# Optimization experiments

Hardware: AMD Instinct MI355X
Metric: run time of the kernel (lower is better)

The kernel has to match this reference:

```python
import jax, jax.numpy as jnp
import numpy as np

H = 8       # num_heads
D = 64      # inner_dim (per-head)
DM = 512    # input_dim == output_dim
EPS = 1e-5


def setup_inputs() -> dict:
    key = jax.random.key(0)
    ks = jax.random.split(key, 6)
    b, n = 2, 2048
    x = jax.random.normal(ks[0], (b, n, DM), dtype=jnp.float32)
    w_qkv = jax.random.normal(ks[1], (DM, 3 * H * D), dtype=jnp.float32) * (DM ** -0.5)
    head_mix = jax.random.normal(ks[2], (H, H), dtype=jnp.float32)
    ln_h_g = jnp.ones((H,), jnp.float32)
    ln_h_b = jnp.zeros((H,), jnp.float32)
    w_out = jax.random.normal(ks[3], (H * D, DM), dtype=jnp.float32) * ((H * D) ** -0.5)
    b_out = jnp.zeros((DM,), jnp.float32)
    ln_o_g = jnp.ones((DM,), jnp.float32)
    ln_o_b = jnp.zeros((DM,), jnp.float32)
    return {"x": x, "w_qkv": w_qkv, "head_mix": head_mix,
            "ln_h_g": ln_h_g, "ln_h_b": ln_h_b,
            "w_out": w_out, "b_out": b_out,
            "ln_o_g": ln_o_g, "ln_o_b": ln_o_b}


def reference(x, w_qkv, head_mix, ln_h_g, ln_h_b, w_out, b_out, ln_o_g, ln_o_b):
    b, n, _ = x.shape
    scale = D ** -0.5
    qkv = x @ w_qkv                                   # [b, n, 3*H*D]
    q, k, v = jnp.split(qkv, 3, axis=-1)
    def heads(t):
        return t.reshape(b, n, H, D).transpose(0, 2, 1, 3)  # [b, H, n, D]
    q, k, v = heads(q), heads(k), heads(v)
    dots = jnp.einsum('bhid,bhjd->bhij', q, k) * scale
    attn = jax.nn.softmax(dots, axis=-1)
    # talking-heads mix: bhij,hg->bgij
    attn = jnp.einsum('bhij,hg->bgij', attn, head_mix)
    # LayerNorm over the head axis (axis=1)
    mu = attn.mean(axis=1, keepdims=True)
    var = attn.var(axis=1, keepdims=True)
    attn = (attn - mu) * jax.lax.rsqrt(var + EPS)
    attn = attn * ln_h_g[None, :, None, None] + ln_h_b[None, :, None, None]
    out = jnp.einsum('bhij,bhjd->bhid', attn, v)      # [b, H, n, D]
    out = out.transpose(0, 2, 1, 3).reshape(b, n, H * D)
    out = out @ w_out + b_out                         # [b, n, DM]
    # LayerNorm over feature dim
    mo = out.mean(axis=-1, keepdims=True)
    vo = out.var(axis=-1, keepdims=True)
    out = (out - mo) * jax.lax.rsqrt(vo + EPS) * ln_o_g + ln_o_b
    out = (x + out).sum(axis=1)                       # [b, DM]
    return out, attn
```

## Files before the change

kernel.cpp:

```cpp
#include <hip/hip_runtime.h>
#include <hip/hip_bf16.h>

typedef __attribute__((ext_vector_type(8)))  short short8;
typedef __attribute__((ext_vector_type(16))) float f32x16;

#define LOG2E 1.44269504088896f
#define CS (0.125f * LOG2E)

static __device__ __forceinline__ short f2b(float f) {
  union { __hip_bfloat16 h; short s; } u; u.h = __float2bfloat16(f); return u.s;
}
static __device__ __forceinline__ f32x16 zf16() {
  f32x16 z;
#pragma unroll
  for (int i = 0; i < 16; ++i) z[i] = 0.f;
  return z;
}
static __device__ __forceinline__ f32x16 mfma32(short8 a, short8 b, f32x16 c) {
  return __builtin_amdgcn_mfma_f32_32x32x16_bf16(a, b, c, 0, 0, 0);
}
static __device__ __forceinline__ float rfl(float v) {
  return __int_as_float(__builtin_amdgcn_readfirstlane(__float_as_int(v)));
}

__global__ void k_convert(const float* __restrict__ x, const float* __restrict__ wqkv,
                          const float* __restrict__ wout,
                          short* __restrict__ xb, short* __restrict__ wqkvT,
                          short* __restrict__ woutT) {
  const int NX = 2 * 2048 * 512;
  const int NW = 512 * 1536;
  const int NO = 512 * 512;
  int i = blockIdx.x * 256 + threadIdx.x;
  if (i < NX) {
    xb[i] = f2b(x[i]);
  } else if (i < NX + NW) {
    int o = i - NX; int n = o >> 9; int k = o & 511;
    wqkvT[o] = f2b(wqkv[k * 1536 + n]);
  } else if (i < NX + NW + NO) {
    int o = i - NX - NW; int n = o >> 9; int k = o & 511;
    woutT[o] = f2b(wout[k * 512 + n]);
  }
}

__global__ void k_xsum(const float* __restrict__ x, float* __restrict__ outacc) {
  int blk = blockIdx.x;
  int b = blk >> 4, ch = blk & 15;
  int t = threadIdx.x;
  int f = t * 2;
  float s0 = 0.f, s1 = 0.f;
  const float* base = x + ((size_t)b * 2048 + (size_t)ch * 128) * 512;
  for (int r = 0; r < 128; ++r) {
    float2 v = *(const float2*)(base + (size_t)r * 512 + f);
    s0 += v.x; s1 += v.y;
  }
  atomicAdd(&outacc[b * 512 + f], s0);
  atomicAdd(&outacc[b * 512 + f + 1], s1);
}

__launch_bounds__(256)
__global__ void k_qkv(const short* __restrict__ xb, const short* __restrict__ wqkvT,
                      short* __restrict__ qg, short* __restrict__ kg,
                      short* __restrict__ vtmp) {
  __shared__ __align__(16) short As[128 * 64];
  __shared__ __align__(16) short Bs[128 * 64];
  int bx = blockIdx.x & 31;
  int by = blockIdx.x >> 5;
  int row0 = bx << 7, col0 = by << 7;
  int t = threadIdx.x, w = t >> 6, l = t & 63, li = l & 31, hi = l >> 5;
  int wr = w >> 1, wc = w & 1;
  f32x16 acc[2][2];
#pragma unroll
  for (int mi = 0; mi < 2; ++mi)
#pragma unroll
    for (int ni = 0; ni < 2; ++ni) acc[mi][ni] = zf16();

  for (int k0 = 0; k0 < 512; k0 += 64) {
    __syncthreads();
#pragma unroll
    for (int it = 0; it < 4; ++it) {
      int idx = t + it * 256;
      int r = idx >> 3, pc = idx & 7;
      int4 va = *(const int4*)(xb + (size_t)(row0 + r) * 512 + k0 + pc * 8);
      int dsto = (r * 128 + pc * 16) ^ ((r & 7) << 4);
      *(int4*)((char*)As + dsto) = va;
      int4 vb = *(const int4*)(wqkvT + (size_t)(col0 + r) * 512 + k0 + pc * 8);
      *(int4*)((char*)Bs + dsto) = vb;
    }
    __syncthreads();
#pragma unroll
    for (int kk = 0; kk < 4; ++kk) {
      short8 af[2], bfv[2];
#pragma unroll
      for (int mi = 0; mi < 2; ++mi) {
        int row = wr * 64 + mi * 32 + li;
        int byteo = (row * 128 + (kk * 2 + hi) * 16) ^ ((row & 7) << 4);
        af[mi] = *(const short8*)((char*)As + byteo);
      }
#pragma unroll
      for (int ni = 0; ni < 2; ++ni) {
        int col = wc * 64 + ni * 32 + li;
        int byteo = (col * 128 + (kk * 2 + hi) * 16) ^ ((col & 7) << 4);
        bfv[ni] = *(const short8*)((char*)Bs + byteo);
      }
#pragma unroll
      for (int mi = 0; mi < 2; ++mi)
#pragma unroll
        for (int ni = 0; ni < 2; ++ni)
          acc[mi][ni] = mfma32(af[mi], bfv[ni], acc[mi][ni]);
    }
  }
#pragma unroll
  for (int mi = 0; mi < 2; ++mi)
#pragma unroll
    for (int ni = 0; ni < 2; ++ni) {
      int colb = col0 + wc * 64 + ni * 32 + li;
      int sect = colb >> 9, rem = colb & 511, h = rem >> 6, d = rem & 63;
      short* dst = sect == 0 ? qg : (sect == 1 ? kg : vtmp);
#pragma unroll
      for (int r = 0; r < 16; ++r) {
        int row = row0 + wr * 64 + mi * 32 + ((r & 3) + ((r >> 2) << 3) + (hi << 2));
        int b = row >> 11, nn = row & 2047;
        dst[(((size_t)(b * 8 + h) * 2048 + nn) << 6) + d] = f2b(acc[mi][ni][r]);
      }
    }
}

__global__ void k_vt(const short* __restrict__ vtmp, short* __restrict__ vt) {
  __shared__ __align__(16) short tile[64 * 72];
  int blk = blockIdx.x;
  int bh = blk >> 5;
  int n0 = (blk & 31) << 6;
  int t = threadIdx.x;
#pragma unroll
  for (int it = 0; it < 2; ++it) {
    int idx = (t + it * 256) * 8;
    int r = idx >> 6, c = idx & 63;
    int4 v = *(const int4*)(vtmp + ((size_t)bh * 2048 + n0 + r) * 64 + c);
    *(int4*)(&tile[r * 72 + c]) = v;
  }
  __syncthreads();
#pragma unroll
  for (int it = 0; it < 2; ++it) {
    int idx = (t + it * 256) * 8;
    int d = idx >> 6, nn = idx & 63;
    short8 o;
#pragma unroll
    for (int j = 0; j < 8; ++j) o[j] = tile[(nn + j) * 72 + d];
    *(short8*)(vt + ((size_t)bh * 64 + d) * 2048 + n0 + nn) = o;
  }
}

__launch_bounds__(256)
__global__ void k_stats(const short* __restrict__ qg, const short* __restrict__ kg,
                        float* __restrict__ ml) {
  __shared__ float red[4][32][2];
  int t = threadIdx.x, w = t >> 6, l = t & 63, li = l & 31, hi = l >> 5;
  int blk = blockIdx.x;
  int b = blk >> 9, rem = blk & 511, h = rem >> 6, it = rem & 63;
  size_t bh = (size_t)(b * 8 + h) * 2048;
  int i = it * 32 + li;
  short8 q4[4];
#pragma unroll
  for (int kk = 0; kk < 4; ++kk)
    q4[kk] = *(const short8*)(qg + (bh + i) * 64 + kk * 16 + hi * 8);
  float m2 = -1e30f, ls = 0.f;
  for (int jt = w * 16; jt < w * 16 + 16; ++jt) {
    f32x16 s = zf16();
#pragma unroll
    for (int kk = 0; kk < 4; ++kk) {
      short8 kf = *(const short8*)(kg + (bh + jt * 32 + li) * 64 + kk * 16 + hi * 8);
      s = mfma32(kf, q4[kk], s);
    }
    float sv[16];
    float tm = -1e30f;
#pragma unroll
    for (int r = 0; r < 16; ++r) { sv[r] = s[r] * CS; tm = fmaxf(tm, sv[r]); }
    float mn = fmaxf(m2, tm);
    float acc = 0.f;
#pragma unroll
    for (int r = 0; r < 16; ++r) acc += exp2f(sv[r] - mn);
    ls = ls * exp2f(m2 - mn) + acc;
    m2 = mn;
  }
  float om = __shfl_xor(m2, 32, 64);
  float ol = __shfl_xor(ls, 32, 64);
  float mf = fmaxf(m2, om);
  float lf = ls * exp2f(m2 - mf) + ol * exp2f(om - mf);
  if (hi == 0) { red[w][li][0] = mf; red[w][li][1] = lf; }
  __syncthreads();
  if (t < 32) {
    float m = red[0][t][0], s = red[0][t][1];
#pragma unroll
    for (int ww = 1; ww < 4; ++ww) {
      float m1 = red[ww][t][0], s1 = red[ww][t][1];
      float mn = fmaxf(m, m1);
      s = s * exp2f(m - mn) + s1 * exp2f(m1 - mn);
      m = mn;
    }
    *(float2*)(ml + (bh + it * 32 + t) * 2) = make_float2(m, s);
  }
}

__launch_bounds__(512, 4)
__global__ void k_attn(const short* __restrict__ qg, const short* __restrict__ kg,
                       const short* __restrict__ vt, const float* __restrict__ ml,
                       const float* __restrict__ mixg, const float* __restrict__ lnhg,
                       const float* __restrict__ lnhb, float* __restrict__ attn,
                       float* __restrict__ oh) {
  __shared__ __align__(16) float p_lds[8 * 32 * 33];
  __shared__ __align__(16) short a_lds[8 * 32 * 40];
  int t = threadIdx.x;
  int w = t >> 6, l = t & 63, li = l & 31, hi = l >> 5;
  int blk = blockIdx.x;
  int jg = blk & 3, itile = (blk >> 2) & 63, b = blk >> 8;
  int i0 = itile * 32;
  int h = w;
  size_t bh = (size_t)(b * 8 + h) * 2048;

  float mixr[64];
#pragma unroll
  for (int z = 0; z < 64; ++z) mixr[z] = rfl(mixg[z]);
  float lg[8], lbv[8];
#pragma unroll
  for (int g = 0; g < 8; ++g) { lg[g] = rfl(lnhg[g]); lbv[g] = rfl(lnhb[g]); }

  short8 q4[4];
#pragma unroll
  for (int kk = 0; kk < 4; ++kk)
    q4[kk] = *(const short8*)(qg + (bh + i0 + li) * 64 + kk * 16 + hi * 8);
  float2 mlv = *(const float2*)(ml + (bh + i0 + li) * 2);
  float c0 = -(mlv.x + __log2f(mlv.y));

  f32x16 oacc[2];
  oacc[0] = zf16(); oacc[1] = zf16();

  int ii = t >> 4;
  int jp = (t & 15) * 2;

  for (int jt = 0; jt < 16; ++jt) {
    int j0 = jg * 512 + jt * 32;
    f32x16 s = zf16();
#pragma unroll
    for (int kk = 0; kk < 4; ++kk) {
      short8 kf = *(const short8*)(kg + (bh + j0 + li) * 64 + kk * 16 + hi * 8);
      s = mfma32(kf, q4[kk], s);
    }
#pragma unroll
    for (int r = 0; r < 16; ++r) {
      float p = exp2f(fmaf(s[r], CS, c0));
      int jr = (r & 3) + ((r >> 2) << 3) + (hi << 2);
      p_lds[(h * 32 + jr) * 33 + li] = p;
    }
    __syncthreads();
    {
      float pf[8][2], a[8][2];
#pragma unroll
      for (int g = 0; g < 8; ++g) {
        pf[g][0] = p_lds[(g * 32 + jp) * 33 + ii];
        pf[g][1] = p_lds[(g * 32 + jp + 1) * 33 + ii];
      }
#pragma unroll
      for (int g = 0; g < 8; ++g) {
#pragma unroll
        for (int jb = 0; jb < 2; ++jb) {
          float a2 = 0.f;
#pragma unroll
          for (int hh = 0; hh < 8; ++hh) a2 = fmaf(pf[hh][jb], mixr[hh * 8 + g], a2);
          a[g][jb] = a2;
        }
      }
      float mu[2], rs[2];
#pragma unroll
      for (int jb = 0; jb < 2; ++jb) {
        float m2 = 0.f;
#pragma unroll
        for (int g = 0; g < 8; ++g) m2 += a[g][jb];
        m2 *= 0.125f;
        float var = 0.f;
#pragma unroll
        for (int g = 0; g < 8; ++g) { float d2 = a[g][jb] - m2; var = fmaf(d2, d2, var); }
        var *= 0.125f;
        mu[jb] = m2; rs[jb] = rsqrtf(var + 1e-5f);
      }
#pragma unroll
      for (int g = 0; g < 8; ++g) {
        float y0 = (a[g][0] - mu[0]) * rs[0] * lg[g] + lbv[g];
        float y1 = (a[g][1] - mu[1]) * rs[1] * lg[g] + lbv[g];
        *(float2*)(&attn[((size_t)(b * 8 + g) * 2048 + (size_t)(i0 + ii)) * 2048 + j0 + jp]) =
            make_float2(y0, y1);
        unsigned int pk = (unsigned short)f2b(y0) | ((unsigned int)(unsigned short)f2b(y1) << 16);
        *(unsigned int*)(&a_lds[(g * 32 + ii) * 40 + jp]) = pk;
      }
    }
    __syncthreads();
#pragma unroll
    for (int ks = 0; ks < 2; ++ks) {
      short8 af = *(const short8*)(&a_lds[(h * 32 + li) * 40 + ks * 16 + hi * 8]);
#pragma unroll
      for (int dt = 0; dt < 2; ++dt) {
        short8 vf = *(const short8*)(vt + ((size_t)(b * 8 + h) * 64 + dt * 32 + li) * 2048 + j0 + ks * 16 + hi * 8);
        oacc[dt] = mfma32(af, vf, oacc[dt]);
      }
    }
  }
  float* ohp = oh + (size_t)jg * (2 * 2048 * 512);
#pragma unroll
  for (int dt = 0; dt < 2; ++dt)
#pragma unroll
    for (int r = 0; r < 16; ++r) {
      int ri = (r & 3) + ((r >> 2) << 3) + (hi << 2);
      ohp[((size_t)(b * 2048 + i0 + ri)) * 512 + h * 64 + dt * 32 + li] = oacc[dt][r];
    }
}

__launch_bounds__(512)
__global__ void k_epi(const float* __restrict__ oh, const short* __restrict__ woutT,
                      const float* __restrict__ bo, const float* __restrict__ logv,
                      const float* __restrict__ lob, float* __restrict__ dout) {
  __shared__ __align__(16) short As[32 * 64];
  __shared__ float lnsum[32][8];
  __shared__ float lnsq[32][8];
  __shared__ float zsum[512];
  const size_t NPART = (size_t)2 * 2048 * 512;
  int t = threadIdx.x, w = t >> 6, l = t & 63, li = l & 31, hi = l >> 5;
  int m0 = blockIdx.x * 32;
  f32x16 acc[2];
  acc[0] = zf16(); acc[1] = zf16();

  for (int k0 = 0; k0 < 512; k0 += 64) {
    __syncthreads();
    {
      int r = t >> 4, c = (t & 15) * 4;
      size_t off = (size_t)(m0 + r) * 512 + k0 + c;
      float4 v = *(const float4*)(oh + off);
#pragma unroll
      for (int p = 1; p < 4; ++p) {
        float4 v2 = *(const float4*)(oh + p * NPART + off);
        v.x += v2.x; v.y += v2.y; v.z += v2.z; v.w += v2.w;
      }
      short o[4] = { f2b(v.x), f2b(v.y), f2b(v.z), f2b(v.w) };
      int byteo = (r * 128 + c * 2) ^ ((r & 7) << 4);
      *(int2*)((char*)As + byteo) = *(int2*)o;
    }
    __syncthreads();
#pragma unroll
    for (int kk = 0; kk < 4; ++kk) {
      int byteo = (li * 128 + (kk * 2 + hi) * 16) ^ ((li & 7) << 4);
      short8 af = *(const short8*)((char*)As + byteo);
#pragma unroll
      for (int ni = 0; ni < 2; ++ni) {
        int n = w * 64 + ni * 32 + li;
        short8 bfr = *(const short8*)(woutT + (size_t)n * 512 + k0 + kk * 16 + hi * 8);
        acc[ni] = mfma32(af, bfr, acc[ni]);
      }
    }
  }
  float bias[2], gg[2], b2[2];
#pragma unroll
  for (int ni = 0; ni < 2; ++ni) {
    int n = w * 64 + ni * 32 + li;
    bias[ni] = bo[n]; gg[ni] = logv[n]; b2[ni] = lob[n];
  }
#pragma unroll
  for (int ni = 0; ni < 2; ++ni)
#pragma unroll
    for (int r = 0; r < 16; ++r) acc[ni][r] += bias[ni];

#pragma unroll
  for (int r = 0; r < 16; ++r) {
    float s = acc[0][r] + acc[1][r];
    float q2 = fmaf(acc[0][r], acc[0][r], acc[1][r] * acc[1][r]);
    for (int d2 = 1; d2 < 32; d2 <<= 1) { s += __shfl_xor(s, d2); q2 += __shfl_xor(q2, d2); }
    int row = (r & 3) + ((r >> 2) << 3) + (hi << 2);
    if (li == 0) { lnsum[row][w] = s; lnsq[row][w] = q2; }
  }
  __syncthreads();
  if (t < 32) {
    float s = 0.f, q2 = 0.f;
#pragma unroll
    for (int ww = 0; ww < 8; ++ww) { s += lnsum[t][ww]; q2 += lnsq[t][ww]; }
    float m2 = s * (1.f / 512.f);
    float var = q2 * (1.f / 512.f) - m2 * m2;
    lnsum[t][0] = m2;
    lnsq[t][0] = rsqrtf(var + 1e-5f);
  }
  __syncthreads();
  float zc[2] = {0.f, 0.f};
#pragma unroll
  for (int r = 0; r < 16; ++r) {
    int row = (r & 3) + ((r >> 2) << 3) + (hi << 2);
    float m2 = lnsum[row][0], rs = lnsq[row][0];
#pragma unroll
    for (int ni = 0; ni < 2; ++ni)
      zc[ni] += (acc[ni][r] - m2) * rs * gg[ni] + b2[ni];
  }
#pragma unroll
  for (int ni = 0; ni < 2; ++ni) zc[ni] += __shfl_xor(zc[ni], 32);
  if (hi == 0) {
#pragma unroll
    for (int ni = 0; ni < 2; ++ni) zsum[w * 64 + ni * 32 + li] = zc[ni];
  }
  __syncthreads();
  int bsel = m0 >> 11;
  atomicAdd(&dout[bsel * 512 + t], zsum[t]);
}

extern "C" void kernel_launch(void* const* d_in, const int* in_sizes, int n_in,
                              void* d_out, int out_size, void* d_ws, size_t ws_size,
                              hipStream_t stream) {
  const float* x    = (const float*)d_in[0];
  const float* wqkv = (const float*)d_in[1];
  const float* mixg = (const float*)d_in[2];
  const float* lnhg = (const float*)d_in[3];
  const float* lnhb = (const float*)d_in[4];
  const float* wout = (const float*)d_in[5];
  const float* bo   = (const float*)d_in[6];
  const float* logv = (const float*)d_in[7];
  const float* lob  = (const float*)d_in[8];
  float* dout = (float*)d_out;
  char* ws = (char*)d_ws;
  short* xb    = (short*)(ws + 0);
  short* wqkvT = (short*)(ws + 4194304);
  short* woutT = (short*)(ws + 5767168);
  short* qg    = (short*)(ws + 6291456);
  short* kg    = (short*)(ws + 10485760);
  short* vtmp  = (short*)(ws + 14680064);
  short* vt    = (short*)(ws + 18874368);
  float* ml    = (float*)(ws + 23068672);
  float* oh    = (float*)(ws + 23330816);

  hipMemsetAsync(dout, 0, 1024 * sizeof(float), stream);

  k_convert<<<12288, 256, 0, stream>>>(x, wqkv, wout, xb, wqkvT, woutT);
  k_xsum<<<32, 256, 0, stream>>>(x, dout);
  k_qkv<<<384, 256, 0, stream>>>(xb, wqkvT, qg, kg, vtmp);
  k_vt<<<512, 256, 0, stream>>>(vtmp, vt);
  k_stats<<<1024, 256, 0, stream>>>(qg, kg, ml);
  k_attn<<<512, 512, 0, stream>>>(qg, kg, vt, ml, mixg, lnhg, lnhb, dout + 1024, oh);
  k_epi<<<128, 512, 0, stream>>>(oh, woutT, bo, logv, lob, dout);
}
```

Baseline: 452.4 us.

## Compute talking-heads mix with MFMA on bf16 probabilities instead of scalar FMAs

Replaces the per-thread 8x8 scalar head-mixing (64 FMAs per element with 64 mix registers) with a 32x32x16 bf16 MFMA, where the mix matrix sits in the first 8 rows of the A operand and the probabilities are stored as bf16 in swizzled LDS. The head LayerNorm is then computed with a cross-half shuffle, and the occupancy hint in launch_bounds is dropped because register pressure should fall. The intent is to remove the VALU and register cost of the mix. In exchange, most of the MFMA work is zero padding, probabilities are rounded to bf16 before mixing, which loses precision, and the attn stores become scalar 4-byte writes instead of float2.

Result: slower. 493.2 us (+9.0%).

```diff
diff --git a/kernel.cpp b/kernel.cpp
--- a/kernel.cpp
+++ b/kernel.cpp
@@ -18,9 +18,6 @@
 }
 static __device__ __forceinline__ f32x16 mfma32(short8 a, short8 b, f32x16 c) {
   return __builtin_amdgcn_mfma_f32_32x32x16_bf16(a, b, c, 0, 0, 0);
-}
-static __device__ __forceinline__ float rfl(float v) {
-  return __int_as_float(__builtin_amdgcn_readfirstlane(__float_as_int(v)));
 }
 
 __global__ void k_convert(const float* __restrict__ x, const float* __restrict__ wqkv,
@@ -201,13 +198,13 @@
   }
 }
 
-__launch_bounds__(512, 4)
+__launch_bounds__(512)
 __global__ void k_attn(const short* __restrict__ qg, const short* __restrict__ kg,
                        const short* __restrict__ vt, const float* __restrict__ ml,
                        const float* __restrict__ mixg, const float* __restrict__ lnhg,
                        const float* __restrict__ lnhb, float* __restrict__ attn,
                        float* __restrict__ oh) {
-  __shared__ __align__(16) float p_lds[8 * 32 * 33];
+  __shared__ __align__(16) short p_lds[1024 * 8];
   __shared__ __align__(16) short a_lds[8 * 32 * 40];
   int t = threadIdx.x;
   int w = t >> 6, l = t & 63, li = l & 31, hi = l >> 5;
@@ -217,12 +214,13 @@
   int h = w;
   size_t bh = (size_t)(b * 8 + h) * 2048;
 
-  float mixr[64];
-#pragma unroll
-  for (int z = 0; z < 64; ++z) mixr[z] = rfl(mixg[z]);
-  float lg[8], lbv[8];
-#pragma unroll
-  for (int g = 0; g < 8; ++g) { lg[g] = rfl(lnhg[g]); lbv[g] = rfl(lnhb[g]); }
+  short8 mixA;
+#pragma unroll
+  for (int e = 0; e < 8; ++e)
+    mixA[e] = (hi == 0 && li < 8) ? f2b(mixg[e * 8 + li]) : (short)0;
+  float lg4[4], lb4[4];
+#pragma unroll
+  for (int e = 0; e < 4; ++e) { lg4[e] = lnhg[4 * hi + e]; lb4[e] = lnhb[4 * hi + e]; }
 
   short8 q4[4];
 #pragma unroll
@@ -234,9 +232,6 @@
   f32x16 oacc[2];
   oacc[0] = zf16(); oacc[1] = zf16();
 
-  int ii = t >> 4;
-  int jp = (t & 15) * 2;
-
   for (int jt = 0; jt < 16; ++jt) {
     int j0 = jg * 512 + jt * 32;
     f32x16 s = zf16();
@@ -249,47 +244,44 @@
     for (int r = 0; r < 16; ++r) {
       float p = exp2f(fmaf(s[r], CS, c0));
       int jr = (r & 3) + ((r >> 2) << 3) + (hi << 2);
-      p_lds[(h * 32 + jr) * 33 + li] = p;
-    }
-    __syncthreads();
-    {
-      float pf[8][2], a[8][2];
-#pragma unroll
-      for (int g = 0; g < 8; ++g) {
-        pf[g][0] = p_lds[(g * 32 + jp) * 33 + ii];
-        pf[g][1] = p_lds[(g * 32 + jp + 1) * 33 + ii];
-      }
-#pragma unroll
-      for (int g = 0; g < 8; ++g) {
-#pragma unroll
-        for (int jb = 0; jb < 2; ++jb) {
-          float a2 = 0.f;
-#pragma unroll
-          for (int hh = 0; hh < 8; ++hh) a2 = fmaf(pf[hh][jb], mixr[hh * 8 + g], a2);
-          a[g][jb] = a2;
-        }
-      }
-      float mu[2], rs[2];
-#pragma unroll
-      for (int jb = 0; jb < 2; ++jb) {
-        float m2 = 0.f;
-#pragma unroll
-        for (int g = 0; g < 8; ++g) m2 += a[g][jb];
-        m2 *= 0.125f;
-        float var = 0.f;
-#pragma unroll
-        for (int g = 0; g < 8; ++g) { float d2 = a[g][jb] - m2; var = fmaf(d2, d2, var); }
-        var *= 0.125f;
-        mu[jb] = m2; rs[jb] = rsqrtf(var + 1e-5f);
-      }
-#pragma unroll
-      for (int g = 0; g < 8; ++g) {
-        float y0 = (a[g][0] - mu[0]) * rs[0] * lg[g] + lbv[g];
-        float y1 = (a[g][1] - mu[1]) * rs[1] * lg[g] + lbv[g];
-        *(float2*)(&attn[((size_t)(b * 8 + g) * 2048 + (size_t)(i0 + ii)) * 2048 + j0 + jp]) =
-            make_float2(y0, y1);
-        unsigned int pk = (unsigned short)f2b(y0) | ((unsigned int)(unsigned short)f2b(y1) << 16);
-        *(unsigned int*)(&a_lds[(g * 32 + ii) * 40 + jp]) = pk;
+      int c = li * 32 + jr;
+      int byteo = (c * 16 + h * 2) ^ ((li & 7) << 4);
+      *(short*)((char*)p_lds + byteo) = f2b(p);
+    }
+    __syncthreads();
+#pragma unroll
+    for (int mm = 0; mm < 4; ++mm) {
+      int m = w * 4 + mm;
+      short8 pB;
+      if (hi == 0) {
+        int byteo = (m * 512 + li * 16) ^ ((m & 7) << 4);
+        pB = *(const short8*)((char*)p_lds + byteo);
+      } else {
+#pragma unroll
+        for (int e = 0; e < 8; ++e) pB[e] = 0;
+      }
+      f32x16 macc = mfma32(mixA, pB, zf16());
+      float a4[4], o4[4];
+#pragma unroll
+      for (int e = 0; e < 4; ++e) { a4[e] = macc[e]; o4[e] = __shfl_xor(macc[e], 32, 64); }
+      float mu = 0.f;
+#pragma unroll
+      for (int e = 0; e < 4; ++e) mu += a4[e] + o4[e];
+      mu *= 0.125f;
+      float var = 0.f;
+#pragma unroll
+      for (int e = 0; e < 4; ++e) {
+        float d1 = a4[e] - mu, d2 = o4[e] - mu;
+        var = fmaf(d1, d1, var); var = fmaf(d2, d2, var);
+      }
+      var *= 0.125f;
+      float rs = rsqrtf(var + 1e-5f);
+#pragma unroll
+      for (int e = 0; e < 4; ++e) {
+        float y = (a4[e] - mu) * rs * lg4[e] + lb4[e];
+        int g = 4 * hi + e;
+        attn[((size_t)(b * 8 + g) * 2048 + (size_t)(i0 + m)) * 2048 + j0 + li] = y;
+        a_lds[(g * 32 + m) * 40 + li] = f2b(y);
       }
     }
     __syncthreads();
```
